# Kernel optimization log

Hardware: AMD Instinct MI355X
Metric: run time of the kernel (lower is better)

Reference implementation:

```python
import jax, jax.numpy as jnp
import numpy as np

FP16_HUGE = 2.0 ** 15
NUM_HEAD = 4
LN_EPS = 1e-5


def setup_inputs() -> dict:
    key = jax.random.key(0)
    ks = jax.random.split(key, 12)
    B, N, D = 1, 256, 128
    H = NUM_HEAD
    inp = {
        "pair_act": jax.random.normal(ks[0], (B, N, N, D), dtype=jnp.float32),
        "pair_mask": jnp.ones((B, N, N), dtype=jnp.float32),
        "ln_scale": jnp.ones((D,), dtype=jnp.float32),
        "ln_bias": jnp.zeros((D,), dtype=jnp.float32),
        # torch Linear weight layout: [out_dim, in_dim]; applied as x @ W.T
        "w2d": jax.random.normal(ks[1], (H, D), dtype=jnp.float32) / np.sqrt(D),
        "wq": jax.random.normal(ks[2], (D, D), dtype=jnp.float32) / np.sqrt(D),
        "wk": jax.random.normal(ks[3], (D, D), dtype=jnp.float32) / np.sqrt(D),
        "wv": jax.random.normal(ks[4], (D, D), dtype=jnp.float32) / np.sqrt(D),
        "wg": jax.random.normal(ks[5], (D, D), dtype=jnp.float32) / np.sqrt(D),
        "bg": jnp.ones((D,), dtype=jnp.float32),  # gating bias init = 1.0
        "wo": jax.random.normal(ks[6], (D, D), dtype=jnp.float32) * 0.02,
        "bo": jnp.zeros((D,), dtype=jnp.float32),
    }
    return inp


def reference(pair_act, pair_mask, ln_scale, ln_bias, w2d, wq, wk, wv, wg, bg, wo, bo):
    B, N, _, D = pair_act.shape
    H = NUM_HEAD
    kd = D // H  # per-head key/value dim
    scale = kd ** (-0.5)

    # mask bias: [B, N(row), 1, 1, N(key)]
    bias = (FP16_HUGE * (pair_mask - 1.0))[:, :, None, None, :]

    # LayerNorm (fp32, eps=1e-5)
    mu = jnp.mean(pair_act, axis=-1, keepdims=True)
    var = jnp.mean(jnp.square(pair_act - mu), axis=-1, keepdims=True)
    x = (pair_act - mu) * jax.lax.rsqrt(var + LN_EPS) * ln_scale + ln_bias

    # non-batched per-head bias: [B, 1, H, N, N]
    nb = jnp.einsum("bijd,hd->bhij", x, w2d)[:, None]

    q = (x @ wq.T).reshape(B, N, N, H, kd) * scale  # [B, r, i, H, kd]
    k = (x @ wk.T).reshape(B, N, N, H, kd)
    v = (x @ wv.T).reshape(B, N, N, H, kd)

    logits = jnp.einsum("brihk,brjhk->brhij", q, k) + bias + nb  # [B, r, H, i, j]
    w = jax.nn.softmax(logits, axis=-1)
    o = jnp.einsum("brhij,brjhv->brihv", w, v)  # [B, r, i, H, kd]

    g = jax.nn.sigmoid(x @ wg.T + bg).reshape(B, N, N, H, kd)
    o = (o * g).reshape(B, N, N, D)

    out = o @ wo.T + bo
    return out * pair_mask[..., None]
```

## Files before the change

### kernel.cpp

```cpp
#include <hip/hip_runtime.h>
#include <hip/hip_bf16.h>

typedef unsigned short u16;
typedef __attribute__((ext_vector_type(8))) short bf16x8;
typedef __attribute__((ext_vector_type(4))) float f32x4;
typedef __attribute__((address_space(3))) unsigned lds_u32;
typedef const __attribute__((address_space(1))) unsigned glb_u32;

#define N 256
#define D 128
#define NH 4
#define KD 32
#define NN 65536
#define QK_SCALE 0.17677669529663687f
#define LOG2E 1.4426950408889634f
#define HUGE_MASK 32768.0f

__device__ __forceinline__ float b2f(u16 s) {
  union { float f; unsigned u; } x; x.u = ((unsigned)s) << 16; return x.f;
}
__device__ __forceinline__ u16 f2b(float f) {
  union { float f; unsigned u; } x; x.f = f;
  unsigned r = x.u + 0x7fff + ((x.u >> 16) & 1);
  return (u16)(r >> 16);
}
__device__ __forceinline__ float exp2v(float x) {
  float r; __asm__("v_exp_f32 %0, %1" : "=v"(r) : "v"(x)); return r;
}

__global__ __launch_bounds__(256) void prep_w_kernel(
    const float* __restrict__ wq, const float* __restrict__ wk,
    const float* __restrict__ wv, const float* __restrict__ wg,
    const float* __restrict__ wo, u16* __restrict__ wb)
{
  int idx = blockIdx.x * 256 + threadIdx.x;
  const float* srcs[5] = {wq, wk, wv, wg, wo};
  int mat = idx >> 11, rem = idx & 2047;
  int row = rem >> 4, g = rem & 15;
  int gp = (g + (row & 15)) & 15;
  const float* s = srcs[mat] + row * 128 + g * 8;
  float4 f0 = *(const float4*)(s);
  float4 f1 = *(const float4*)(s + 4);
  uint4 pk;
  pk.x = (unsigned)f2b(f0.x) | ((unsigned)f2b(f0.y) << 16);
  pk.y = (unsigned)f2b(f0.z) | ((unsigned)f2b(f0.w) << 16);
  pk.z = (unsigned)f2b(f1.x) | ((unsigned)f2b(f1.y) << 16);
  pk.w = (unsigned)f2b(f1.z) | ((unsigned)f2b(f1.w) << 16);
  *(uint4*)(wb + (size_t)mat * 16384 + row * 128 + gp * 8) = pk;
}

__device__ __forceinline__ void async_stage(const u16* __restrict__ gsrc, u16* lds, int tid) {
  int lane = tid & 63, wave = tid >> 6;
  u16* lbase = lds + wave * 512;
  const u16* gbase = gsrc + wave * 512 + lane * 8;
#pragma unroll
  for (int p = 0; p < 8; p++) {
    __builtin_amdgcn_global_load_lds((glb_u32*)(gbase + p * 2048),
                                     (lds_u32*)(lbase + p * 2048), 16, 0, 0);
  }
}

__global__ __launch_bounds__(256) void projln_kernel(
    const float* __restrict__ pa, const float* __restrict__ lns, const float* __restrict__ lnb,
    const float* __restrict__ w2d, const u16* __restrict__ wb, const float* __restrict__ bg,
    u16* __restrict__ q, u16* __restrict__ k, u16* __restrict__ v, u16* __restrict__ g,
    float* __restrict__ nb)
{
  __shared__ __align__(16) u16 Wl[2][16384];
  int tid = threadIdx.x;
  int wave = tid >> 6, lane = tid & 63;
  int lr = lane & 15, quad = lane >> 4;

  async_stage(wb, Wl[0], tid);

  bf16x8 a[2][4];
#pragma unroll
  for (int mt = 0; mt < 2; mt++) {
    int row = blockIdx.x * 128 + wave * 32 + mt * 16 + lr;
    const float* rp = pa + (size_t)row * D;
    float xv[4][8];
    float s = 0.f, ss = 0.f;
#pragma unroll
    for (int ks = 0; ks < 4; ks++) {
      float4 a0 = *(const float4*)(rp + ks * 32 + quad * 8);
      float4 a1 = *(const float4*)(rp + ks * 32 + quad * 8 + 4);
      xv[ks][0] = a0.x; xv[ks][1] = a0.y; xv[ks][2] = a0.z; xv[ks][3] = a0.w;
      xv[ks][4] = a1.x; xv[ks][5] = a1.y; xv[ks][6] = a1.z; xv[ks][7] = a1.w;
#pragma unroll
      for (int j = 0; j < 8; j++) { s += xv[ks][j]; ss += xv[ks][j] * xv[ks][j]; }
    }
    s  += __shfl_xor(s, 16, 64);  ss += __shfl_xor(ss, 16, 64);
    s  += __shfl_xor(s, 32, 64);  ss += __shfl_xor(ss, 32, 64);
    float mu = s * (1.0f / D);
    float var = ss * (1.0f / D) - mu * mu;
    float rs = rsqrtf(var + 1e-5f);
#pragma unroll
    for (int ks = 0; ks < 4; ks++) {
      float4 s0 = *(const float4*)(lns + ks * 32 + quad * 8);
      float4 s1 = *(const float4*)(lns + ks * 32 + quad * 8 + 4);
      float4 b0 = *(const float4*)(lnb + ks * 32 + quad * 8);
      float4 b1 = *(const float4*)(lnb + ks * 32 + quad * 8 + 4);
      float sc[8] = {s0.x,s0.y,s0.z,s0.w,s1.x,s1.y,s1.z,s1.w};
      float bi[8] = {b0.x,b0.y,b0.z,b0.w,b1.x,b1.y,b1.z,b1.w};
#pragma unroll
      for (int j = 0; j < 8; j++) xv[ks][j] = (xv[ks][j] - mu) * rs * sc[j] + bi[j];
    }
#pragma unroll
    for (int h = 0; h < NH; h++) {
      float p = 0.f;
#pragma unroll
      for (int ks = 0; ks < 4; ks++) {
        float4 w0 = *(const float4*)(w2d + h * D + ks * 32 + quad * 8);
        float4 w1 = *(const float4*)(w2d + h * D + ks * 32 + quad * 8 + 4);
        p += xv[ks][0]*w0.x + xv[ks][1]*w0.y + xv[ks][2]*w0.z + xv[ks][3]*w0.w
           + xv[ks][4]*w1.x + xv[ks][5]*w1.y + xv[ks][6]*w1.z + xv[ks][7]*w1.w;
      }
      p += __shfl_xor(p, 16, 64);
      p += __shfl_xor(p, 32, 64);
      if (quad == 0)
        nb[(size_t)h * NN + row] = p * LOG2E;
    }
#pragma unroll
    for (int ks = 0; ks < 4; ks++)
#pragma unroll
      for (int j = 0; j < 8; j++) a[mt][ks][j] = (short)f2b(xv[ks][j]);
  }
  __syncthreads();

  u16* Os[4] = {q, k, v, g};
#pragma unroll
  for (int mat = 0; mat < 4; mat++) {
    if (mat < 3) async_stage(wb + (size_t)(mat + 1) * 16384, Wl[(mat + 1) & 1], tid);
    const u16* Wcur = Wl[mat & 1];
    f32x4 acc[2][2][4];
#pragma unroll
    for (int mt = 0; mt < 2; mt++)
#pragma unroll
      for (int tg = 0; tg < 2; tg++)
#pragma unroll
        for (int e = 0; e < 4; e++) acc[mt][tg][e] = (f32x4){0.f, 0.f, 0.f, 0.f};
#pragma unroll
    for (int ks = 0; ks < 4; ks++) {
#pragma unroll
      for (int tg = 0; tg < 2; tg++) {
#pragma unroll
        for (int e = 0; e < 4; e++) {
          int nrow = tg * 64 + 4 * lr + e;
          int gp = (ks * 4 + quad + (nrow & 15)) & 15;
          bf16x8 b = *(const bf16x8*)(&Wcur[nrow * 128 + gp * 8]);
          acc[0][tg][e] = __builtin_amdgcn_mfma_f32_16x16x32_bf16(a[0][ks], b, acc[0][tg][e], 0, 0, 0);
          acc[1][tg][e] = __builtin_amdgcn_mfma_f32_16x16x32_bf16(a[1][ks], b, acc[1][tg][e], 0, 0, 0);
        }
      }
    }
    u16* O = Os[mat];
#pragma unroll
    for (int mt = 0; mt < 2; mt++) {
      int row0 = blockIdx.x * 128 + wave * 32 + mt * 16 + quad * 4;
#pragma unroll
      for (int tg = 0; tg < 2; tg++) {
        int c0 = tg * 64 + 4 * lr;
        float bg0 = 0.f, bg1 = 0.f, bg2 = 0.f, bg3 = 0.f;
        if (mat == 3) { bg0 = bg[c0]; bg1 = bg[c0+1]; bg2 = bg[c0+2]; bg3 = bg[c0+3]; }
#pragma unroll
        for (int reg = 0; reg < 4; reg++) {
          float v0 = acc[mt][tg][0][reg], v1 = acc[mt][tg][1][reg];
          float v2 = acc[mt][tg][2][reg], v3 = acc[mt][tg][3][reg];
          if (mat == 0) {
            v0 *= QK_SCALE * LOG2E; v1 *= QK_SCALE * LOG2E;
            v2 *= QK_SCALE * LOG2E; v3 *= QK_SCALE * LOG2E;
          }
          if (mat == 3) {
            v0 = 1.0f / (1.0f + __expf(-(v0 + bg0)));
            v1 = 1.0f / (1.0f + __expf(-(v1 + bg1)));
            v2 = 1.0f / (1.0f + __expf(-(v2 + bg2)));
            v3 = 1.0f / (1.0f + __expf(-(v3 + bg3)));
          }
          uint2 pk;
          pk.x = (unsigned)f2b(v0) | ((unsigned)f2b(v1) << 16);
          pk.y = (unsigned)f2b(v2) | ((unsigned)f2b(v3) << 16);
          *(uint2*)(O + (size_t)(row0 + reg) * D + c0) = pk;
        }
      }
    }
    __syncthreads();
  }
}

__global__ __launch_bounds__(256) void attn_kernel(
    const u16* __restrict__ q, const u16* __restrict__ k, const u16* __restrict__ v,
    const u16* __restrict__ g, const float* __restrict__ nb, const float* __restrict__ mask,
    u16* __restrict__ og)
{
  __shared__ __align__(16) u16 Kf[8192];
  __shared__ __align__(16) u16 Vf[8192];
  __shared__ float bias_lds[256];
  int h = blockIdx.x & 3, r = blockIdx.x >> 2;
  int tid = threadIdx.x;
  {
    int j = tid;
    const u16* krow = k + ((size_t)r * N + j) * D + h * KD;
    int t = j >> 4, lrj = j & 15;
#pragma unroll
    for (int qc = 0; qc < 4; qc++)
      *(bf16x8*)(&Kf[((t * 4 + qc) * 16 + lrj) * 8]) = *(const bf16x8*)(krow + qc * 8);
    const u16* vrow = v + ((size_t)r * N + j) * D + h * KD;
    int ksrc = j >> 5, jrel = j & 31;
    int qv, jv;
    if (jrel < 16) { qv = jrel >> 2; jv = jrel & 3; }
    else           { qv = (jrel & 15) >> 2; jv = 4 + (jrel & 3); }
#pragma unroll
    for (int c = 0; c < 32; c++)
      Vf[(((ksrc * 2 + (c & 1)) * 4 + qv) * 16 + (c >> 1)) * 8 + jv] = vrow[c];
    bias_lds[tid] = (HUGE_MASK * LOG2E) * (mask[r * N + tid] - 1.0f);
  }
  __syncthreads();
  int wave = tid >> 6, lane = tid & 63;
  int lr = lane & 15, quad = lane >> 4;
  const float* nbh = nb + (size_t)h * NN;

  for (int pass = 0; pass < 4; pass++) {
    int i0 = pass * 64 + wave * 16;
    int irow = i0 + lr;
    bf16x8 af = *(const bf16x8*)(q + ((size_t)r * N + irow) * D + h * KD + quad * 8);
    const float* nbrow = nbh + (size_t)irow * N;
    float m = 0.f, ls = 0.f;
    f32x4 oa = (f32x4){0.f,0.f,0.f,0.f}, ob = (f32x4){0.f,0.f,0.f,0.f};
#pragma unroll 1
    for (int c = 0; c < 2; c++) {
      f32x4 S[8];
#pragma unroll
      for (int tt = 0; tt < 8; tt++) {
        int t = c * 8 + tt;
        int jb = t * 16 + quad * 4;
        float4 nb4 = *(const float4*)(nbrow + jb);
        float4 b4  = *(const float4*)(&bias_lds[jb]);
        f32x4 ci;
        ci[0] = nb4.x + b4.x; ci[1] = nb4.y + b4.y;
        ci[2] = nb4.z + b4.z; ci[3] = nb4.w + b4.w;
        bf16x8 kfr = *(const bf16x8*)(&Kf[((t * 4 + quad) * 16 + lr) * 8]);
        S[tt] = __builtin_amdgcn_mfma_f32_16x16x32_bf16(kfr, af, ci, 0, 0, 0);
      }
      float m0 = -3e38f, m1 = -3e38f, m2 = -3e38f, m3 = -3e38f;
#pragma unroll
      for (int tt = 0; tt < 8; tt++) {
        m0 = fmaxf(m0, S[tt][0]); m1 = fmaxf(m1, S[tt][1]);
        m2 = fmaxf(m2, S[tt][2]); m3 = fmaxf(m3, S[tt][3]);
      }
      float ma = fmaxf(fmaxf(m0, m1), fmaxf(m2, m3));
      ma = fmaxf(ma, __shfl_xor(ma, 16, 64));
      ma = fmaxf(ma, __shfl_xor(ma, 32, 64));
      if (c == 0) {
        m = ma;
      } else {
        float mnew = fmaxf(m, ma);
        float sc = exp2v(m - mnew);
        m = mnew;
        ls *= sc;
        float s0 = __shfl(sc, quad * 4 + 0, 64);
        float s1 = __shfl(sc, quad * 4 + 1, 64);
        float s2 = __shfl(sc, quad * 4 + 2, 64);
        float s3 = __shfl(sc, quad * 4 + 3, 64);
        oa[0] *= s0; oa[1] *= s1; oa[2] *= s2; oa[3] *= s3;
        ob[0] *= s0; ob[1] *= s1; ob[2] *= s2; ob[3] *= s3;
      }
#pragma unroll
      for (int kk = 0; kk < 4; kk++) {
        int ks = c * 4 + kk;
        float p0 = exp2v(S[2*kk][0] - m);
        float p1 = exp2v(S[2*kk][1] - m);
        float p2 = exp2v(S[2*kk][2] - m);
        float p3 = exp2v(S[2*kk][3] - m);
        float p4 = exp2v(S[2*kk+1][0] - m);
        float p5 = exp2v(S[2*kk+1][1] - m);
        float p6 = exp2v(S[2*kk+1][2] - m);
        float p7 = exp2v(S[2*kk+1][3] - m);
        ls += ((p0 + p1) + (p2 + p3)) + ((p4 + p5) + (p6 + p7));
        union { bf16x8 v; unsigned u[4]; } pa;
        __asm__("v_cvt_pk_bf16_f32 %0, %1, %2" : "=v"(pa.u[0]) : "v"(p0), "v"(p1));
        __asm__("v_cvt_pk_bf16_f32 %0, %1, %2" : "=v"(pa.u[1]) : "v"(p2), "v"(p3));
        __asm__("v_cvt_pk_bf16_f32 %0, %1, %2" : "=v"(pa.u[2]) : "v"(p4), "v"(p5));
        __asm__("v_cvt_pk_bf16_f32 %0, %1, %2" : "=v"(pa.u[3]) : "v"(p6), "v"(p7));
        bf16x8 vb0 = *(const bf16x8*)(&Vf[(((ks * 2 + 0) * 4 + quad) * 16 + lr) * 8]);
        oa = __builtin_amdgcn_mfma_f32_16x16x32_bf16(pa.v, vb0, oa, 0, 0, 0);
        bf16x8 vb1 = *(const bf16x8*)(&Vf[(((ks * 2 + 1) * 4 + quad) * 16 + lr) * 8]);
        ob = __builtin_amdgcn_mfma_f32_16x16x32_bf16(pa.v, vb1, ob, 0, 0, 0);
      }
    }
    float lsum = ls;
    lsum += __shfl_xor(lsum, 16, 64);
    lsum += __shfl_xor(lsum, 32, 64);
    float invd = __builtin_amdgcn_rcpf(lsum);

#pragma unroll
    for (int reg = 0; reg < 4; reg++) {
      float inv = __shfl(invd, quad * 4 + reg, 64);
      int i = i0 + quad * 4 + reg;
      size_t base = ((size_t)r * N + i) * D + h * KD + 2 * lr;
      unsigned gv = *(const unsigned*)(g + base);
      float r0 = oa[reg] * inv * b2f((u16)(gv & 0xffff));
      float r1 = ob[reg] * inv * b2f((u16)(gv >> 16));
      *(unsigned*)(og + base) = (unsigned)f2b(r0) | ((unsigned)f2b(r1) << 16);
    }
  }
}

__global__ __launch_bounds__(256) void out_kernel(
    const u16* __restrict__ og, const u16* __restrict__ wob, const float* __restrict__ bo,
    const float* __restrict__ mask, float* __restrict__ out)
{
  __shared__ __align__(16) u16 Wlds[16384];
  int tid = threadIdx.x;
  async_stage(wob, Wlds, tid);
  int wave = tid >> 6, lane = tid & 63;
  int lr = lane & 15, quad = lane >> 4;
  bf16x8 a[2][4];
#pragma unroll
  for (int mt = 0; mt < 2; mt++) {
    int arow = blockIdx.x * 128 + wave * 32 + mt * 16 + lr;
#pragma unroll
    for (int ks = 0; ks < 4; ks++)
      a[mt][ks] = *(const bf16x8*)(og + (size_t)arow * D + ks * 32 + quad * 8);
  }
  __syncthreads();
  f32x4 acc[2][2][4];
#pragma unroll
  for (int mt = 0; mt < 2; mt++)
#pragma unroll
    for (int tg = 0; tg < 2; tg++)
#pragma unroll
      for (int e = 0; e < 4; e++) acc[mt][tg][e] = (f32x4){0.f, 0.f, 0.f, 0.f};
#pragma unroll
  for (int ks = 0; ks < 4; ks++) {
#pragma unroll
    for (int tg = 0; tg < 2; tg++) {
#pragma unroll
      for (int e = 0; e < 4; e++) {
        int nrow = tg * 64 + 4 * lr + e;
        int gp = (ks * 4 + quad + (nrow & 15)) & 15;
        bf16x8 b = *(const bf16x8*)(&Wlds[nrow * 128 + gp * 8]);
        acc[0][tg][e] = __builtin_amdgcn_mfma_f32_16x16x32_bf16(a[0][ks], b, acc[0][tg][e], 0, 0, 0);
        acc[1][tg][e] = __builtin_amdgcn_mfma_f32_16x16x32_bf16(a[1][ks], b, acc[1][tg][e], 0, 0, 0);
      }
    }
  }
#pragma unroll
  for (int mt = 0; mt < 2; mt++) {
    int row0 = blockIdx.x * 128 + wave * 32 + mt * 16 + quad * 4;
#pragma unroll
    for (int tg = 0; tg < 2; tg++) {
      int c0 = tg * 64 + 4 * lr;
      float4 bo4 = *(const float4*)(bo + c0);
#pragma unroll
      for (int reg = 0; reg < 4; reg++) {
        int pos = row0 + reg;
        float m = mask[pos];
        float4 o4;
        o4.x = (acc[mt][tg][0][reg] + bo4.x) * m;
        o4.y = (acc[mt][tg][1][reg] + bo4.y) * m;
        o4.z = (acc[mt][tg][2][reg] + bo4.z) * m;
        o4.w = (acc[mt][tg][3][reg] + bo4.w) * m;
        *(float4*)(out + (size_t)pos * D + c0) = o4;
      }
    }
  }
}

extern "C" void kernel_launch(void* const* d_in, const int* in_sizes, int n_in,
                              void* d_out, int out_size, void* d_ws, size_t ws_size,
                              hipStream_t stream)
{
  const float* pa   = (const float*)d_in[0];
  const float* mask = (const float*)d_in[1];
  const float* lns  = (const float*)d_in[2];
  const float* lnb  = (const float*)d_in[3];
  const float* w2d  = (const float*)d_in[4];
  const float* wq   = (const float*)d_in[5];
  const float* wk   = (const float*)d_in[6];
  const float* wv   = (const float*)d_in[7];
  const float* wg   = (const float*)d_in[8];
  const float* bg   = (const float*)d_in[9];
  const float* wo   = (const float*)d_in[10];
  const float* bo   = (const float*)d_in[11];

  const size_t ARR = (size_t)NN * D;
  u16* q  = (u16*)d_ws;
  u16* k  = q + ARR;
  u16* v  = k + ARR;
  u16* g  = v + ARR;
  u16* og = g + ARR;
  float* nb = (float*)(og + ARR);
  u16* wb = (u16*)(nb + (size_t)NH * NN);

  prep_w_kernel<<<40, 256, 0, stream>>>(wq, wk, wv, wg, wo, wb);
  projln_kernel<<<512, 256, 0, stream>>>(pa, lns, lnb, w2d, wb, bg, q, k, v, g, nb);
  attn_kernel<<<N * NH, 256, 0, stream>>>(q, k, v, g, nb, mask, og);
  out_kernel<<<512, 256, 0, stream>>>(og, wb + 4 * 16384, bo, mask, (float*)d_out);
}
```

Baseline: 186.7 us.

## Double wave count per block so each wave handles one 16-row tile

All three main kernels now launch 512 threads (8 waves) instead of 256. Each wave computes a single 16-row M tile instead of two, which halves per-thread accumulator and A-fragment registers, and the LDS weight staging is split across 8 waves. In the attention kernel, K staging is done by half the threads and V staging is split between the two halves, with two passes of 128 query rows instead of four of 64. The aim is more waves in flight to hide latency, at the cost of each weight fragment read from LDS being reused across fewer MFMAs per wave.

```diff
diff --git a/kernel.cpp b/kernel.cpp
--- a/kernel.cpp
+++ b/kernel.cpp
@@ -49,18 +49,18 @@
   *(uint4*)(wb + (size_t)mat * 16384 + row * 128 + gp * 8) = pk;
 }
 
+template <int NW>
 __device__ __forceinline__ void async_stage(const u16* __restrict__ gsrc, u16* lds, int tid) {
   int lane = tid & 63, wave = tid >> 6;
-  u16* lbase = lds + wave * 512;
-  const u16* gbase = gsrc + wave * 512 + lane * 8;
-#pragma unroll
-  for (int p = 0; p < 8; p++) {
-    __builtin_amdgcn_global_load_lds((glb_u32*)(gbase + p * 2048),
-                                     (lds_u32*)(lbase + p * 2048), 16, 0, 0);
-  }
-}
-
-__global__ __launch_bounds__(256) void projln_kernel(
+#pragma unroll
+  for (int p = 0; p < 32 / NW; p++) {
+    int c = wave * (32 / NW) + p;
+    __builtin_amdgcn_global_load_lds((glb_u32*)(gsrc + c * 512 + lane * 8),
+                                     (lds_u32*)(lds + c * 512), 16, 0, 0);
+  }
+}
+
+__global__ __launch_bounds__(512) void projln_kernel(
     const float* __restrict__ pa, const float* __restrict__ lns, const float* __restrict__ lnb,
     const float* __restrict__ w2d, const u16* __restrict__ wb, const float* __restrict__ bg,
     u16* __restrict__ q, u16* __restrict__ k, u16* __restrict__ v, u16* __restrict__ g,
@@ -71,12 +71,11 @@
   int wave = tid >> 6, lane = tid & 63;
   int lr = lane & 15, quad = lane >> 4;
 
-  async_stage(wb, Wl[0], tid);
-
-  bf16x8 a[2][4];
-#pragma unroll
-  for (int mt = 0; mt < 2; mt++) {
-    int row = blockIdx.x * 128 + wave * 32 + mt * 16 + lr;
+  async_stage<8>(wb, Wl[0], tid);
+
+  bf16x8 a[4];
+  int row = blockIdx.x * 128 + wave * 16 + lr;
+  {
     const float* rp = pa + (size_t)row * D;
     float xv[4][8];
     float s = 0.f, ss = 0.f;
@@ -123,22 +122,20 @@
 #pragma unroll
     for (int ks = 0; ks < 4; ks++)
 #pragma unroll
-      for (int j = 0; j < 8; j++) a[mt][ks][j] = (short)f2b(xv[ks][j]);
+      for (int j = 0; j < 8; j++) a[ks][j] = (short)f2b(xv[ks][j]);
   }
   __syncthreads();
 
   u16* Os[4] = {q, k, v, g};
 #pragma unroll
   for (int mat = 0; mat < 4; mat++) {
-    if (mat < 3) async_stage(wb + (size_t)(mat + 1) * 16384, Wl[(mat + 1) & 1], tid);
+    if (mat < 3) async_stage<8>(wb + (size_t)(mat + 1) * 16384, Wl[(mat + 1) & 1], tid);
     const u16* Wcur = Wl[mat & 1];
-    f32x4 acc[2][2][4];
-#pragma unroll
-    for (int mt = 0; mt < 2; mt++)
-#pragma unroll
-      for (int tg = 0; tg < 2; tg++)
-#pragma unroll
-        for (int e = 0; e < 4; e++) acc[mt][tg][e] = (f32x4){0.f, 0.f, 0.f, 0.f};
+    f32x4 acc[2][4];
+#pragma unroll
+    for (int tg = 0; tg < 2; tg++)
+#pragma unroll
+      for (int e = 0; e < 4; e++) acc[tg][e] = (f32x4){0.f, 0.f, 0.f, 0.f};
 #pragma unroll
     for (int ks = 0; ks < 4; ks++) {
 #pragma unroll
@@ -148,46 +145,42 @@
           int nrow = tg * 64 + 4 * lr + e;
           int gp = (ks * 4 + quad + (nrow & 15)) & 15;
           bf16x8 b = *(const bf16x8*)(&Wcur[nrow * 128 + gp * 8]);
-          acc[0][tg][e] = __builtin_amdgcn_mfma_f32_16x16x32_bf16(a[0][ks], b, acc[0][tg][e], 0, 0, 0);
-          acc[1][tg][e] = __builtin_amdgcn_mfma_f32_16x16x32_bf16(a[1][ks], b, acc[1][tg][e], 0, 0, 0);
+          acc[tg][e] = __builtin_amdgcn_mfma_f32_16x16x32_bf16(a[ks], b, acc[tg][e], 0, 0, 0);
         }
       }
     }
     u16* O = Os[mat];
-#pragma unroll
-    for (int mt = 0; mt < 2; mt++) {
-      int row0 = blockIdx.x * 128 + wave * 32 + mt * 16 + quad * 4;
-#pragma unroll
-      for (int tg = 0; tg < 2; tg++) {
-        int c0 = tg * 64 + 4 * lr;
-        float bg0 = 0.f, bg1 = 0.f, bg2 = 0.f, bg3 = 0.f;
-        if (mat == 3) { bg0 = bg[c0]; bg1 = bg[c0+1]; bg2 = bg[c0+2]; bg3 = bg[c0+3]; }
-#pragma unroll
-        for (int reg = 0; reg < 4; reg++) {
-          float v0 = acc[mt][tg][0][reg], v1 = acc[mt][tg][1][reg];
-          float v2 = acc[mt][tg][2][reg], v3 = acc[mt][tg][3][reg];
-          if (mat == 0) {
-            v0 *= QK_SCALE * LOG2E; v1 *= QK_SCALE * LOG2E;
-            v2 *= QK_SCALE * LOG2E; v3 *= QK_SCALE * LOG2E;
-          }
-          if (mat == 3) {
-            v0 = 1.0f / (1.0f + __expf(-(v0 + bg0)));
-            v1 = 1.0f / (1.0f + __expf(-(v1 + bg1)));
-            v2 = 1.0f / (1.0f + __expf(-(v2 + bg2)));
-            v3 = 1.0f / (1.0f + __expf(-(v3 + bg3)));
-          }
-          uint2 pk;
-          pk.x = (unsigned)f2b(v0) | ((unsigned)f2b(v1) << 16);
-          pk.y = (unsigned)f2b(v2) | ((unsigned)f2b(v3) << 16);
-          *(uint2*)(O + (size_t)(row0 + reg) * D + c0) = pk;
+    int row0 = blockIdx.x * 128 + wave * 16 + quad * 4;
+#pragma unroll
+    for (int tg = 0; tg < 2; tg++) {
+      int c0 = tg * 64 + 4 * lr;
+      float bg0 = 0.f, bg1 = 0.f, bg2 = 0.f, bg3 = 0.f;
+      if (mat == 3) { bg0 = bg[c0]; bg1 = bg[c0+1]; bg2 = bg[c0+2]; bg3 = bg[c0+3]; }
+#pragma unroll
+      for (int reg = 0; reg < 4; reg++) {
+        float v0 = acc[tg][0][reg], v1 = acc[tg][1][reg];
+        float v2 = acc[tg][2][reg], v3 = acc[tg][3][reg];
+        if (mat == 0) {
+          v0 *= QK_SCALE * LOG2E; v1 *= QK_SCALE * LOG2E;
+          v2 *= QK_SCALE * LOG2E; v3 *= QK_SCALE * LOG2E;
         }
+        if (mat == 3) {
+          v0 = 1.0f / (1.0f + __expf(-(v0 + bg0)));
+          v1 = 1.0f / (1.0f + __expf(-(v1 + bg1)));
+          v2 = 1.0f / (1.0f + __expf(-(v2 + bg2)));
+          v3 = 1.0f / (1.0f + __expf(-(v3 + bg3)));
+        }
+        uint2 pk;
+        pk.x = (unsigned)f2b(v0) | ((unsigned)f2b(v1) << 16);
+        pk.y = (unsigned)f2b(v2) | ((unsigned)f2b(v3) << 16);
+        *(uint2*)(O + (size_t)(row0 + reg) * D + c0) = pk;
       }
     }
     __syncthreads();
   }
 }
 
-__global__ __launch_bounds__(256) void attn_kernel(
+__global__ __launch_bounds__(512) void attn_kernel(
     const u16* __restrict__ q, const u16* __restrict__ k, const u16* __restrict__ v,
     const u16* __restrict__ g, const float* __restrict__ nb, const float* __restrict__ mask,
     u16* __restrict__ og)
@@ -198,29 +191,34 @@
   int h = blockIdx.x & 3, r = blockIdx.x >> 2;
   int tid = threadIdx.x;
   {
-    int j = tid;
-    const u16* krow = k + ((size_t)r * N + j) * D + h * KD;
-    int t = j >> 4, lrj = j & 15;
-#pragma unroll
-    for (int qc = 0; qc < 4; qc++)
-      *(bf16x8*)(&Kf[((t * 4 + qc) * 16 + lrj) * 8]) = *(const bf16x8*)(krow + qc * 8);
+    int j = tid & 255;
+    if (tid < 256) {
+      const u16* krow = k + ((size_t)r * N + j) * D + h * KD;
+      int t = j >> 4, lrj = j & 15;
+#pragma unroll
+      for (int qc = 0; qc < 4; qc++)
+        *(bf16x8*)(&Kf[((t * 4 + qc) * 16 + lrj) * 8]) = *(const bf16x8*)(krow + qc * 8);
+      bias_lds[j] = (HUGE_MASK * LOG2E) * (mask[r * N + j] - 1.0f);
+    }
     const u16* vrow = v + ((size_t)r * N + j) * D + h * KD;
     int ksrc = j >> 5, jrel = j & 31;
     int qv, jv;
     if (jrel < 16) { qv = jrel >> 2; jv = jrel & 3; }
     else           { qv = (jrel & 15) >> 2; jv = 4 + (jrel & 3); }
-#pragma unroll
-    for (int c = 0; c < 32; c++)
+    int chalf = (tid >> 8) * 16;
+#pragma unroll
+    for (int cc = 0; cc < 16; cc++) {
+      int c = chalf + cc;
       Vf[(((ksrc * 2 + (c & 1)) * 4 + qv) * 16 + (c >> 1)) * 8 + jv] = vrow[c];
-    bias_lds[tid] = (HUGE_MASK * LOG2E) * (mask[r * N + tid] - 1.0f);
+    }
   }
   __syncthreads();
   int wave = tid >> 6, lane = tid & 63;
   int lr = lane & 15, quad = lane >> 4;
   const float* nbh = nb + (size_t)h * NN;
 
-  for (int pass = 0; pass < 4; pass++) {
-    int i0 = pass * 64 + wave * 16;
+  for (int pp = 0; pp < 2; pp++) {
+    int i0 = pp * 128 + wave * 16;
     int irow = i0 + lr;
     bf16x8 af = *(const bf16x8*)(q + ((size_t)r * N + irow) * D + h * KD + quad * 8);
     const float* nbrow = nbh + (size_t)irow * N;
@@ -305,31 +303,26 @@
   }
 }
 
-__global__ __launch_bounds__(256) void out_kernel(
+__global__ __launch_bounds__(512) void out_kernel(
     const u16* __restrict__ og, const u16* __restrict__ wob, const float* __restrict__ bo,
     const float* __restrict__ mask, float* __restrict__ out)
 {
   __shared__ __align__(16) u16 Wlds[16384];
   int tid = threadIdx.x;
-  async_stage(wob, Wlds, tid);
+  async_stage<8>(wob, Wlds, tid);
   int wave = tid >> 6, lane = tid & 63;
   int lr = lane & 15, quad = lane >> 4;
-  bf16x8 a[2][4];
-#pragma unroll
-  for (int mt = 0; mt < 2; mt++) {
-    int arow = blockIdx.x * 128 + wave * 32 + mt * 16 + lr;
-#pragma unroll
-    for (int ks = 0; ks < 4; ks++)
-      a[mt][ks] = *(const bf16x8*)(og + (size_t)arow * D + ks * 32 + quad * 8);
-  }
+  bf16x8 a[4];
+  int arow = blockIdx.x * 128 + wave * 16 + lr;
+#pragma unroll
+  for (int ks = 0; ks < 4; ks++)
+    a[ks] = *(const bf16x8*)(og + (size_t)arow * D + ks * 32 + quad * 8);
   __syncthreads();
-  f32x4 acc[2][2][4];
-#pragma unroll
-  for (int mt = 0; mt < 2; mt++)
-#pragma unroll
-    for (int tg = 0; tg < 2; tg++)
-#pragma unroll
-      for (int e = 0; e < 4; e++) acc[mt][tg][e] = (f32x4){0.f, 0.f, 0.f, 0.f};
+  f32x4 acc[2][4];
+#pragma unroll
+  for (int tg = 0; tg < 2; tg++)
+#pragma unroll
+    for (int e = 0; e < 4; e++) acc[tg][e] = (f32x4){0.f, 0.f, 0.f, 0.f};
 #pragma unroll
   for (int ks = 0; ks < 4; ks++) {
 #pragma unroll
@@ -339,29 +332,25 @@
         int nrow = tg * 64 + 4 * lr + e;
         int gp = (ks * 4 + quad + (nrow & 15)) & 15;
         bf16x8 b = *(const bf16x8*)(&Wlds[nrow * 128 + gp * 8]);
-        acc[0][tg][e] = __builtin_amdgcn_mfma_f32_16x16x32_bf16(a[0][ks], b, acc[0][tg][e], 0, 0, 0);
-        acc[1][tg][e] = __builtin_amdgcn_mfma_f32_16x16x32_bf16(a[1][ks], b, acc[1][tg][e], 0, 0, 0);
-      }
-    }
-  }
-#pragma unroll
-  for (int mt = 0; mt < 2; mt++) {
-    int row0 = blockIdx.x * 128 + wave * 32 + mt * 16 + quad * 4;
-#pragma unroll
-    for (int tg = 0; tg < 2; tg++) {
-      int c0 = tg * 64 + 4 * lr;
-      float4 bo4 = *(const float4*)(bo + c0);
-#pragma unroll
-      for (int reg = 0; reg < 4; reg++) {
-        int pos = row0 + reg;
-        float m = mask[pos];
-        float4 o4;
-        o4.x = (acc[mt][tg][0][reg] + bo4.x) * m;
-        o4.y = (acc[mt][tg][1][reg] + bo4.y) * m;
-        o4.z = (acc[mt][tg][2][reg] + bo4.z) * m;
-        o4.w = (acc[mt][tg][3][reg] + bo4.w) * m;
-        *(float4*)(out + (size_t)pos * D + c0) = o4;
-      }
+        acc[tg][e] = __builtin_amdgcn_mfma_f32_16x16x32_bf16(a[ks], b, acc[tg][e], 0, 0, 0);
+      }
+    }
+  }
+  int row0 = blockIdx.x * 128 + wave * 16 + quad * 4;
+#pragma unroll
+  for (int tg = 0; tg < 2; tg++) {
+    int c0 = tg * 64 + 4 * lr;
+    float4 bo4 = *(const float4*)(bo + c0);
+#pragma unroll
+    for (int reg = 0; reg < 4; reg++) {
+      int pos = row0 + reg;
+      float mk = mask[pos];
+      float4 o4;
+      o4.x = (acc[tg][0][reg] + bo4.x) * mk;
+      o4.y = (acc[tg][1][reg] + bo4.y) * mk;
+      o4.z = (acc[tg][2][reg] + bo4.z) * mk;
+      o4.w = (acc[tg][3][reg] + bo4.w) * mk;
+      *(float4*)(out + (size_t)pos * D + c0) = o4;
     }
   }
 }
@@ -393,7 +382,7 @@
   u16* wb = (u16*)(nb + (size_t)NH * NN);
 
   prep_w_kernel<<<40, 256, 0, stream>>>(wq, wk, wv, wg, wo, wb);
-  projln_kernel<<<512, 256, 0, stream>>>(pa, lns, lnb, w2d, wb, bg, q, k, v, g, nb);
-  attn_kernel<<<N * NH, 256, 0, stream>>>(q, k, v, g, nb, mask, og);
-  out_kernel<<<512, 256, 0, stream>>>(og, wb + 4 * 16384, bo, mask, (float*)d_out);
-}
+  projln_kernel<<<512, 512, 0, stream>>>(pa, lns, lnb, w2d, wb, bg, q, k, v, g, nb);
+  attn_kernel<<<N * NH, 512, 0, stream>>>(q, k, v, g, nb, mask, og);
+  out_kernel<<<512, 512, 0, stream>>>(og, wb + 4 * 16384, bo, mask, (float*)d_out);
+}
```

After: 186.6 us. Within noise of the previous version (-0.1%).
